# Performance work log

Measured on AMD Instinct MI355X. Metric: run time of the kernel, lower is better.

Reference implementation:

```python
import jax, jax.numpy as jnp
import numpy as np

N_ENVS = 8
MIN_SIGMA = 0.01

def setup_inputs() -> dict:
    key = jax.random.key(0)
    ks = jax.random.split(key, 16)
    B, T, d, L, H = 32, 64, 128, 64, 256
    H2 = H // 2
    s = 0.05
    return {
        "z_signal": jax.random.normal(ks[0], (B, T, d, L), dtype=jnp.float32),
        "z_corrupt": jax.random.normal(ks[1], (B, T, d, L), dtype=jnp.float32),
        "A": jax.random.uniform(ks[2], (d, d), dtype=jnp.float32),
        "regime": jax.random.randint(ks[3], (B,), 0, N_ENVS),
        # signal_proj: Linear(L -> H)
        "W_sig": jax.random.normal(ks[4], (L, H), dtype=jnp.float32) * s,
        "b_sig": jnp.zeros((H,), dtype=jnp.float32),
        # per-env mechanisms: Linear(H->H), ReLU, Linear(H->2), stacked over envs
        "W1e": jax.random.normal(ks[5], (N_ENVS, H, H), dtype=jnp.float32) * s,
        "b1e": jnp.zeros((N_ENVS, H), dtype=jnp.float32),
        "W2e": jax.random.normal(ks[6], (N_ENVS, H, 2), dtype=jnp.float32) * s,
        "b2e": jnp.zeros((N_ENVS, 2), dtype=jnp.float32),
        # corrupt path: Linear(L -> H//2), ReLU, Linear(H//2 -> 1)
        "Wc": jax.random.normal(ks[7], (L, H2), dtype=jnp.float32) * s,
        "bc": jnp.zeros((H2,), dtype=jnp.float32),
        "Wo": jax.random.normal(ks[8], (H2, 1), dtype=jnp.float32) * s,
        "bo": jnp.zeros((1,), dtype=jnp.float32),
    }

def reference(z_signal, z_corrupt, A, regime, W_sig, b_sig, W1e, b1e, W2e, b2e, Wc, bc, Wo, bo):
    # z_signal: [B,T,d,L], A: [d,d]
    # z_agg[b,t,i,l] = sum_j A[j,i] * z_signal[b,t,j,l]  (A^T @ z per slice)
    z_agg = jnp.einsum('ji,btjl->btil', A, z_signal)
    h_signal = jnp.einsum('btdl,lh->btdh', z_agg, W_sig) + b_sig  # [B,T,d,H]

    # env dispatch: e_idx = regime if regime < n_envs else 0 (per batch element)
    eidx = jnp.where(regime >= N_ENVS, 0, regime)
    W1 = W1e[eidx]  # [B,H,H]
    b1 = b1e[eidx]  # [B,H]
    W2 = W2e[eidx]  # [B,H,2]
    b2 = b2e[eidx]  # [B,2]

    h1 = jax.nn.relu(jnp.einsum('btdh,bhk->btdk', h_signal, W1) + b1[:, None, None, :])
    out = jnp.einsum('btdh,bhk->btdk', h1, W2) + b2[:, None, None, :]  # [B,T,d,2]
    mu = out[..., 0]
    sigma = jax.nn.softplus(out[..., 1]) + MIN_SIGMA

    # corrupt contribution
    h_c = jnp.einsum('btdl,lh->btdh', z_corrupt, Wc) + bc
    contrib = (jnp.einsum('btdh,ho->btdo', jax.nn.relu(h_c), Wo) + bo)[..., 0]  # [B,T,d]
    mu = mu + contrib
    return mu, sigma
```

## Files before the change

### kernel.cpp

```cpp
#include <hip/hip_runtime.h>
#include <hip/hip_bf16.h>


typedef __attribute__((ext_vector_type(8))) short short8;
typedef __attribute__((ext_vector_type(4))) float f32x4;

#define MFMA16(a, b, c) __builtin_amdgcn_mfma_f32_16x16x32_bf16((a), (b), (c), 0, 0, 0)

__device__ __forceinline__ unsigned short f2bf(float f) {
  union { float f; unsigned u; } v; v.f = f;
  unsigned r = v.u + 0x7fffu + ((v.u >> 16) & 1u);
  return (unsigned short)(r >> 16);
}

__device__ __forceinline__ unsigned pkbf(float a, float b) {
  __hip_bfloat162 t = __float22bfloat162_rn(float2{a, b});
  unsigned u; __builtin_memcpy(&u, &t, 4); return u;
}

__device__ __forceinline__ void gload16(const void* gsrc, void* ldsdst) {
  __builtin_amdgcn_global_load_lds(
      (const __attribute__((address_space(1))) unsigned int*)gsrc,
      (__attribute__((address_space(3))) unsigned int*)ldsdst, 16, 0, 0);
}

__global__ void setup_k(const float* __restrict__ A, const float* __restrict__ W_sig,
                        const float* __restrict__ b_sig, const float* __restrict__ W1e,
                        const float* __restrict__ b1e, const float* __restrict__ W2e,
                        const float* __restrict__ Wc,
                        unsigned short* __restrict__ wsw1f, unsigned short* __restrict__ at_f,
                        unsigned short* __restrict__ wct_f, float* __restrict__ bw) {
  int blk = blockIdx.x, tid = threadIdx.x;
  if (blk < 512) {
    int e = blk >> 6, l = blk & 63, h = tid;
    const float* w1 = W1e + e * 65536 + h;
    const float* ws = W_sig + l * 256;
    float acc = 0.f;
    #pragma unroll 8
    for (int h1 = 0; h1 < 256; ++h1) acc = fmaf(ws[h1], w1[h1 * 256], acc);
    int c = h >> 7, ht = (h >> 4) & 7, col = h & 15;
    int kks = l >> 5, lgl = (l >> 3) & 3, e8 = l & 7;
    int lane = lgl * 16 + col;
    wsw1f[((((e * 2 + c) * 8 + ht) * 2 + kks) * 64 + lane) * 8 + e8] = f2bf(acc);
  } else if (blk < 576) {
    int idx = (blk - 512) * 256 + tid;
    int frag = idx >> 3, e8 = idx & 7;
    int it = frag >> 8, ks = (frag >> 6) & 3, lane = frag & 63;
    int j = ks * 32 + (lane >> 4) * 8 + e8, i = it * 16 + (lane & 15);
    at_f[idx] = f2bf(A[j * 128 + i]);
  } else if (blk < 608) {
    int idx = (blk - 576) * 256 + tid;
    int frag = idx >> 3, e8 = idx & 7;
    int ht = frag >> 7, ks = (frag >> 6) & 1, lane = frag & 63;
    int l = ks * 32 + (lane >> 4) * 8 + e8, h = ht * 16 + (lane & 15);
    wct_f[idx] = f2bf(Wc[l * 128 + h]);
  } else if (blk < 624) {
    int idx = (blk - 608) * 256 + tid;
    int e = idx >> 9, r = idx & 511;
    bw[e * 768 + 256 + r] = W2e[idx];
  } else {
    int e = blk - 624, h = tid;
    const float* w1 = W1e + e * 65536 + h;
    float acc = b1e[e * 256 + h];
    for (int h1 = 0; h1 < 256; ++h1) acc = fmaf(b_sig[h1], w1[h1 * 256], acc);
    bw[e * 768 + h] = acc;
  }
}

__global__ __launch_bounds__(256, 4) void dec_k(
    const float* __restrict__ zs, const float* __restrict__ zcr,
    const int* __restrict__ regime, const float* __restrict__ b2e,
    const float* __restrict__ bc, const float* __restrict__ Wo,
    const float* __restrict__ bo,
    const unsigned short* __restrict__ wsw1f, const unsigned short* __restrict__ at_f,
    const unsigned short* __restrict__ wct_f, const float* __restrict__ bw,
    float* __restrict__ out) {
  __shared__ __align__(16) char sm[37888];
  float* s_bias1 = (float*)(sm + 32768);
  float* s_W2    = s_bias1 + 256;
  float* s_cpart = (float*)(sm + 35840);

  const int bt = ((blockIdx.x & 7) << 8) | (blockIdx.x >> 3);
  const int tid = threadIdx.x;
  const int lane = tid & 63, wave = tid >> 6, lg = lane >> 4, l15 = lane & 15;
  int e = regime[bt >> 6]; if (e >= 8) e = 0;
  const float b2_0 = b2e[2 * e], b2_1 = b2e[2 * e + 1], bo0 = bo[0];

  const float* Z  = zs  + (size_t)bt * 8192;
  const float* Zc = zcr + (size_t)bt * 8192;

  if (wave < 3)
    gload16((const char*)(bw + e * 768) + tid * 16, sm + 32768 + wave * 1024);

  float4 zcv[8];
  #pragma unroll
  for (int k = 0; k < 8; ++k) {
    int g = k * 256 + tid, d = g >> 4, l0 = (g & 15) * 4;
    zcv[k] = *(const float4*)(Zc + d * 64 + l0);
  }
  float4 z0v[4], z1v[4];
  #pragma unroll
  for (int k = 0; k < 4; ++k) {
    int g = k * 256 + tid, j = (g >> 4) * 2, l0 = (g & 15) * 4;
    const float* p = Z + j * 64 + l0;
    z0v[k] = *(const float4*)p;
    z1v[k] = *(const float4*)(p + 64);
  }
  short8 wfr[2][2];
  #pragma unroll
  for (int m = 0; m < 2; ++m)
    #pragma unroll
    for (int ks = 0; ks < 2; ++ks)
      wfr[m][ks] = *(const short8*)(wct_f + ((((wave * 2 + m) * 2 + ks) * 64 + lane) << 3));

  #pragma unroll
  for (int k = 0; k < 8; ++k) {
    int g = k * 256 + tid, d = g >> 4, l0 = (g & 15) * 4;
    unsigned lo = pkbf(zcv[k].x, zcv[k].y);
    unsigned hi = pkbf(zcv[k].z, zcv[k].w);
    int a = (d * 128 + l0 * 2) ^ ((d & 7) << 4);
    *(unsigned long long*)(sm + 16384 + a) = ((unsigned long long)hi << 32) | lo;
  }
  #pragma unroll
  for (int k = 0; k < 4; ++k) {
    int g = k * 256 + tid, j = (g >> 4) * 2, l0 = (g & 15) * 4;
    float a0[4] = {z0v[k].x, z0v[k].y, z0v[k].z, z0v[k].w};
    float a1[4] = {z1v[k].x, z1v[k].y, z1v[k].z, z1v[k].w};
    #pragma unroll
    for (int i2 = 0; i2 < 4; ++i2) {
      int l = l0 + i2;
      unsigned v = pkbf(a0[i2], a1[i2]);
      int a = (l * 256 + j * 2) ^ ((((l >> 2) ^ l) & 7) << 4);
      *(unsigned*)(sm + a) = v;
    }
  }
  __syncthreads();

  short8 abfr[2][4];
  #pragma unroll
  for (int m = 0; m < 2; ++m)
    #pragma unroll
    for (int ks = 0; ks < 4; ++ks)
      abfr[m][ks] = *(const short8*)(at_f + ((((wave * 2 + m) * 4 + ks) * 64 + lane) << 3));
  float4 bcv[2], wov[2];
  #pragma unroll
  for (int m = 0; m < 2; ++m) {
    int hb = (wave * 2 + m) * 16 + lg * 4;
    bcv[m] = *(const float4*)(bc + hb);
    wov[m] = *(const float4*)(Wo + hb);
  }

  float cp[8];
  #pragma unroll
  for (int dt = 0; dt < 8; ++dt) cp[dt] = 0.f;
  #pragma unroll
  for (int dt = 0; dt < 8; ++dt) {
    int brow = dt * 16 + l15;
    short8 bfr0 = *(const short8*)(sm + 16384 + ((brow * 128 + lg * 16) ^ ((brow & 7) << 4)));
    short8 bfr1 = *(const short8*)(sm + 16384 + ((brow * 128 + lg * 16 + 64) ^ ((brow & 7) << 4)));
    #pragma unroll
    for (int m = 0; m < 2; ++m) {
      f32x4 acc = (f32x4){0.f, 0.f, 0.f, 0.f};
      acc = MFMA16(wfr[m][0], bfr0, acc);
      acc = MFMA16(wfr[m][1], bfr1, acc);
      #pragma unroll
      for (int r = 0; r < 4; ++r)
        cp[dt] += fmaxf(acc[r] + bcv[m][r], 0.f) * wov[m][r];
    }
  }
  #pragma unroll
  for (int dt = 0; dt < 8; ++dt) {
    cp[dt] += __shfl_xor(cp[dt], 16);
    cp[dt] += __shfl_xor(cp[dt], 32);
  }
  if (lane < 16) {
    #pragma unroll
    for (int dt = 0; dt < 8; ++dt)
      s_cpart[wave * 128 + dt * 16 + lane] = cp[dt];
  }

  const unsigned short* wse = wsw1f + (size_t)e * 16384;
  short8 wsf0[8][2];
  #pragma unroll
  for (int ht = 0; ht < 8; ++ht)
    #pragma unroll
    for (int ks = 0; ks < 2; ++ks)
      wsf0[ht][ks] = *(const short8*)(wse + (((ht * 2 + ks) * 64 + lane) << 3));

  f32x4 acc1[4][2];
  #pragma unroll
  for (int lt = 0; lt < 4; ++lt)
    #pragma unroll
    for (int m = 0; m < 2; ++m) acc1[lt][m] = (f32x4){0.f, 0.f, 0.f, 0.f};
  #pragma unroll
  for (int ks = 0; ks < 4; ++ks) {
    #pragma unroll
    for (int lt = 0; lt < 4; ++lt) {
      int arow = lt * 16 + l15;
      short8 afr = *(const short8*)(sm + ((arow * 256 + lg * 16 + ks * 64) ^
                                          ((((arow >> 2) ^ arow) & 7) << 4)));
      #pragma unroll
      for (int m = 0; m < 2; ++m) acc1[lt][m] = MFMA16(afr, abfr[m][ks], acc1[lt][m]);
    }
  }
  __syncthreads();

  short8 wsf1[8][2];
  #pragma unroll
  for (int ht = 0; ht < 8; ++ht)
    #pragma unroll
    for (int ks = 0; ks < 2; ++ks)
      wsf1[ht][ks] = *(const short8*)(wse + 8192 + (((ht * 2 + ks) * 64 + lane) << 3));

  #pragma unroll
  for (int lt = 0; lt < 4; ++lt) {
    int l0 = lt * 16 + lg * 4;
    #pragma unroll
    for (int m = 0; m < 2; ++m) {
      int i = (wave * 2 + m) * 16 + l15;
      unsigned lo = pkbf(acc1[lt][m][0], acc1[lt][m][1]);
      unsigned hi = pkbf(acc1[lt][m][2], acc1[lt][m][3]);
      int a = (i * 128 + l0 * 2) ^ ((i & 7) << 4);
      *(unsigned long long*)(sm + 16384 + a) = ((unsigned long long)hi << 32) | lo;
    }
  }
  short8 mbfr[2][2];
  #pragma unroll
  for (int m = 0; m < 2; ++m) {
    int brow = (wave * 2 + m) * 16 + l15;
    #pragma unroll
    for (int ks = 0; ks < 2; ++ks)
      mbfr[m][ks] = *(const short8*)(sm + 16384 +
                       ((brow * 128 + lg * 16 + ks * 64) ^ ((brow & 7) << 4)));
  }

  float v0[2] = {0.f, 0.f}, v1[2] = {0.f, 0.f};
  #pragma unroll
  for (int c = 0; c < 2; ++c) {
    #pragma unroll
    for (int ht = 0; ht < 8; ++ht) {
      int h4 = c * 128 + ht * 16 + lg * 4;
      float4 b1v = *(const float4*)(s_bias1 + h4);
      float4 w2a = *(const float4*)(s_W2 + h4 * 2);
      float4 w2b = *(const float4*)(s_W2 + h4 * 2 + 4);
      #pragma unroll
      for (int m = 0; m < 2; ++m) {
        f32x4 acc = (f32x4){0.f, 0.f, 0.f, 0.f};
        if (c == 0) {
          acc = MFMA16(wsf0[ht][0], mbfr[m][0], acc);
          acc = MFMA16(wsf0[ht][1], mbfr[m][1], acc);
        } else {
          acc = MFMA16(wsf1[ht][0], mbfr[m][0], acc);
          acc = MFMA16(wsf1[ht][1], mbfr[m][1], acc);
        }
        float p0 = fmaxf(acc[0] + b1v.x, 0.f), p1 = fmaxf(acc[1] + b1v.y, 0.f);
        float p2 = fmaxf(acc[2] + b1v.z, 0.f), p3 = fmaxf(acc[3] + b1v.w, 0.f);
        v0[m] = fmaf(p0, w2a.x, fmaf(p1, w2a.z, fmaf(p2, w2b.x, fmaf(p3, w2b.z, v0[m]))));
        v1[m] = fmaf(p0, w2a.y, fmaf(p1, w2a.w, fmaf(p2, w2b.y, fmaf(p3, w2b.w, v1[m]))));
      }
    }
  }
  #pragma unroll
  for (int m = 0; m < 2; ++m) {
    v0[m] += __shfl_xor(v0[m], 16); v0[m] += __shfl_xor(v0[m], 32);
    v1[m] += __shfl_xor(v1[m], 16); v1[m] += __shfl_xor(v1[m], 32);
  }
  if (lane < 16) {
    #pragma unroll
    for (int m = 0; m < 2; ++m) {
      int d = (wave * 2 + m) * 16 + lane;
      float contrib = s_cpart[d] + s_cpart[128 + d] + s_cpart[256 + d] + s_cpart[384 + d];
      float mu = v0[m] + b2_0 + bo0 + contrib;
      float x = v1[m] + b2_1;
      float sg = fmaxf(x, 0.f) + log1pf(expf(-fabsf(x))) + 0.01f;
      out[(size_t)bt * 128 + d] = mu;
      out[262144 + (size_t)bt * 128 + d] = sg;
    }
  }
}

extern "C" void kernel_launch(void* const* d_in, const int* in_sizes, int n_in,
                              void* d_out, int out_size, void* d_ws, size_t ws_size,
                              hipStream_t stream) {
  const float* zs    = (const float*)d_in[0];
  const float* zcr   = (const float*)d_in[1];
  const float* A     = (const float*)d_in[2];
  const int*   reg   = (const int*)d_in[3];
  const float* W_sig = (const float*)d_in[4];
  const float* b_sig = (const float*)d_in[5];
  const float* W1e   = (const float*)d_in[6];
  const float* b1e   = (const float*)d_in[7];
  const float* W2e   = (const float*)d_in[8];
  const float* b2e   = (const float*)d_in[9];
  const float* Wc    = (const float*)d_in[10];
  const float* bcp   = (const float*)d_in[11];
  const float* Wo    = (const float*)d_in[12];
  const float* bo    = (const float*)d_in[13];

  unsigned short* wsw1f = (unsigned short*)d_ws;
  unsigned short* at_f  = wsw1f + 131072;
  unsigned short* wct_f = at_f + 16384;
  float* bw             = (float*)(wct_f + 8192);

  setup_k<<<632, 256, 0, stream>>>(A, W_sig, b_sig, W1e, b1e, W2e, Wc,
                                   wsw1f, at_f, wct_f, bw);
  dec_k<<<2048, 256, 0, stream>>>(zs, zcr, reg, b2e, bcp, Wo, bo,
                                  wsw1f, at_f, wct_f, bw, (float*)d_out);
}
```

Measured before the change: 51.96 us.

## Load corrupt-path B fragments directly from global and repartition work per wave

```diff
diff --git a/kernel.cpp b/kernel.cpp
--- a/kernel.cpp
+++ b/kernel.cpp
@@ -17,6 +17,8 @@
   __hip_bfloat162 t = __float22bfloat162_rn(float2{a, b});
   unsigned u; __builtin_memcpy(&u, &t, 4); return u;
 }
+
+union S8 { short8 s; unsigned u[4]; };
 
 __device__ __forceinline__ void gload16(const void* gsrc, void* ldsdst) {
   __builtin_amdgcn_global_load_lds(
@@ -75,10 +77,9 @@
     const unsigned short* __restrict__ wsw1f, const unsigned short* __restrict__ at_f,
     const unsigned short* __restrict__ wct_f, const float* __restrict__ bw,
     float* __restrict__ out) {
-  __shared__ __align__(16) char sm[37888];
+  __shared__ __align__(16) char sm[35840];
   float* s_bias1 = (float*)(sm + 32768);
   float* s_W2    = s_bias1 + 256;
-  float* s_cpart = (float*)(sm + 35840);
 
   const int bt = ((blockIdx.x & 7) << 8) | (blockIdx.x >> 3);
   const int tid = threadIdx.x;
@@ -92,12 +93,6 @@
   if (wave < 3)
     gload16((const char*)(bw + e * 768) + tid * 16, sm + 32768 + wave * 1024);
 
-  float4 zcv[8];
-  #pragma unroll
-  for (int k = 0; k < 8; ++k) {
-    int g = k * 256 + tid, d = g >> 4, l0 = (g & 15) * 4;
-    zcv[k] = *(const float4*)(Zc + d * 64 + l0);
-  }
   float4 z0v[4], z1v[4];
   #pragma unroll
   for (int k = 0; k < 4; ++k) {
@@ -106,20 +101,16 @@
     z0v[k] = *(const float4*)p;
     z1v[k] = *(const float4*)(p + 64);
   }
-  short8 wfr[2][2];
-  #pragma unroll
-  for (int m = 0; m < 2; ++m)
-    #pragma unroll
-    for (int ks = 0; ks < 2; ++ks)
-      wfr[m][ks] = *(const short8*)(wct_f + ((((wave * 2 + m) * 2 + ks) * 64 + lane) << 3));
-
-  #pragma unroll
-  for (int k = 0; k < 8; ++k) {
-    int g = k * 256 + tid, d = g >> 4, l0 = (g & 15) * 4;
-    unsigned lo = pkbf(zcv[k].x, zcv[k].y);
-    unsigned hi = pkbf(zcv[k].z, zcv[k].w);
-    int a = (d * 128 + l0 * 2) ^ ((d & 7) << 4);
-    *(unsigned long long*)(sm + 16384 + a) = ((unsigned long long)hi << 32) | lo;
+  float4 zq[2][2][2];
+  #pragma unroll
+  for (int q = 0; q < 2; ++q) {
+    int dcol = (wave * 2 + q) * 16 + l15;
+    #pragma unroll
+    for (int ks = 0; ks < 2; ++ks) {
+      const float* p = Zc + dcol * 64 + ks * 32 + lg * 8;
+      zq[q][ks][0] = *(const float4*)p;
+      zq[q][ks][1] = *(const float4*)(p + 4);
+    }
   }
   #pragma unroll
   for (int k = 0; k < 4; ++k) {
@@ -136,47 +127,47 @@
   }
   __syncthreads();
 
+  short8 bq[2][2];
+  #pragma unroll
+  for (int q = 0; q < 2; ++q)
+    #pragma unroll
+    for (int ks = 0; ks < 2; ++ks) {
+      S8 t;
+      t.u[0] = pkbf(zq[q][ks][0].x, zq[q][ks][0].y);
+      t.u[1] = pkbf(zq[q][ks][0].z, zq[q][ks][0].w);
+      t.u[2] = pkbf(zq[q][ks][1].x, zq[q][ks][1].y);
+      t.u[3] = pkbf(zq[q][ks][1].z, zq[q][ks][1].w);
+      bq[q][ks] = t.s;
+    }
+
   short8 abfr[2][4];
   #pragma unroll
   for (int m = 0; m < 2; ++m)
     #pragma unroll
     for (int ks = 0; ks < 4; ++ks)
       abfr[m][ks] = *(const short8*)(at_f + ((((wave * 2 + m) * 4 + ks) * 64 + lane) << 3));
-  float4 bcv[2], wov[2];
-  #pragma unroll
-  for (int m = 0; m < 2; ++m) {
-    int hb = (wave * 2 + m) * 16 + lg * 4;
-    bcv[m] = *(const float4*)(bc + hb);
-    wov[m] = *(const float4*)(Wo + hb);
-  }
-
-  float cp[8];
-  #pragma unroll
-  for (int dt = 0; dt < 8; ++dt) cp[dt] = 0.f;
-  #pragma unroll
-  for (int dt = 0; dt < 8; ++dt) {
-    int brow = dt * 16 + l15;
-    short8 bfr0 = *(const short8*)(sm + 16384 + ((brow * 128 + lg * 16) ^ ((brow & 7) << 4)));
-    short8 bfr1 = *(const short8*)(sm + 16384 + ((brow * 128 + lg * 16 + 64) ^ ((brow & 7) << 4)));
-    #pragma unroll
-    for (int m = 0; m < 2; ++m) {
+
+  float cp[2] = {0.f, 0.f};
+  #pragma unroll
+  for (int ht = 0; ht < 8; ++ht) {
+    short8 wa0 = *(const short8*)(wct_f + (((ht * 2 + 0) * 64 + lane) << 3));
+    short8 wa1 = *(const short8*)(wct_f + (((ht * 2 + 1) * 64 + lane) << 3));
+    float4 bcv = *(const float4*)(bc + ht * 16 + lg * 4);
+    float4 wov = *(const float4*)(Wo + ht * 16 + lg * 4);
+    #pragma unroll
+    for (int q = 0; q < 2; ++q) {
       f32x4 acc = (f32x4){0.f, 0.f, 0.f, 0.f};
-      acc = MFMA16(wfr[m][0], bfr0, acc);
-      acc = MFMA16(wfr[m][1], bfr1, acc);
+      acc = MFMA16(wa0, bq[q][0], acc);
+      acc = MFMA16(wa1, bq[q][1], acc);
       #pragma unroll
       for (int r = 0; r < 4; ++r)
-        cp[dt] += fmaxf(acc[r] + bcv[m][r], 0.f) * wov[m][r];
-    }
-  }
-  #pragma unroll
-  for (int dt = 0; dt < 8; ++dt) {
-    cp[dt] += __shfl_xor(cp[dt], 16);
-    cp[dt] += __shfl_xor(cp[dt], 32);
-  }
-  if (lane < 16) {
-    #pragma unroll
-    for (int dt = 0; dt < 8; ++dt)
-      s_cpart[wave * 128 + dt * 16 + lane] = cp[dt];
+        cp[q] += fmaxf(acc[r] + bcv[r], 0.f) * wov[r];
+    }
+  }
+  #pragma unroll
+  for (int q = 0; q < 2; ++q) {
+    cp[q] += __shfl_xor(cp[q], 16);
+    cp[q] += __shfl_xor(cp[q], 32);
   }
 
   const unsigned short* wse = wsw1f + (size_t)e * 16384;
@@ -265,12 +256,12 @@
     v0[m] += __shfl_xor(v0[m], 16); v0[m] += __shfl_xor(v0[m], 32);
     v1[m] += __shfl_xor(v1[m], 16); v1[m] += __shfl_xor(v1[m], 32);
   }
+
   if (lane < 16) {
     #pragma unroll
     for (int m = 0; m < 2; ++m) {
       int d = (wave * 2 + m) * 16 + lane;
-      float contrib = s_cpart[d] + s_cpart[128 + d] + s_cpart[256 + d] + s_cpart[384 + d];
-      float mu = v0[m] + b2_0 + bo0 + contrib;
+      float mu = v0[m] + b2_0 + bo0 + cp[m];
       float x = v1[m] + b2_1;
       float sg = fmaxf(x, 0.f) + log1pf(expf(-fabsf(x))) + 0.01f;
       out[(size_t)bt * 128 + d] = mu;
```

New measurement: 52.45 us. Within noise of the previous version (+0.9%).
